# Kernel tuning notes

Measured on AMD Instinct MI355X. Metric: run time of the kernel, lower is better.

## Reference

```python
import jax, jax.numpy as jnp
import numpy as np

D, F, E, K = 1024, 2048, 8, 2
EPS = 1.1920929e-07  # torch.finfo(float32).eps, RMSNorm default eps=None


def setup_inputs() -> dict:
    key = jax.random.key(0)
    ks = jax.random.split(key, 6)
    x = jax.random.normal(ks[0], (2, 2048, D), jnp.float32)
    Wg = jax.random.normal(ks[1], (D, E), jnp.float32)          # Gate.weights ~ randn
    norm_w = jnp.ones((E, D), jnp.float32)                       # per-expert RMSNorm weight
    W1 = jax.random.normal(ks[2], (E, D, F), jnp.float32) * 0.02
    b1 = jnp.zeros((E, F), jnp.float32)
    W2 = jax.random.normal(ks[3], (E, D, F), jnp.float32) * 0.02
    b2 = jnp.zeros((E, F), jnp.float32)
    W3 = jax.random.normal(ks[4], (E, F, D), jnp.float32) * 0.02
    b3 = jnp.zeros((E, D), jnp.float32)
    return {"x": x, "Wg": Wg, "norm_w": norm_w, "W1": W1, "b1": b1,
            "W2": W2, "b2": b2, "W3": W3, "b3": b3, "k": K}


def reference(x, Wg, norm_w, W1, b1, W2, b2, W3, b3, k):
    orig_shape = x.shape
    xt = x.reshape(-1, x.shape[-1])                    # [T, d]
    num_experts = Wg.shape[-1]

    # --- Gate: top-k then softmax over selected logits ---
    scores = xt @ Wg                                   # [T, E]
    top_v, top_i = jax.lax.top_k(scores, k)            # [T, k]
    gates = jax.nn.softmax(top_v, axis=-1)             # [T, k]
    # combine weight per (token, expert); zero for unrouted experts
    comb = jnp.einsum('tk,tke->te', gates,
                      jax.nn.one_hot(top_i, num_experts, dtype=gates.dtype))  # [T, E]

    # --- Per-expert SwiGLU FFN with RMSNorm (norm weight folded into W1/W2) ---
    inv = jax.lax.rsqrt(jnp.mean(xt * xt, axis=-1, keepdims=True) + EPS)
    xh = xt * inv                                      # [T, d] (un-weighted RMSNorm)
    W1p = norm_w[:, :, None] * W1                      # [E, d, f]
    W2p = norm_w[:, :, None] * W2
    a = jnp.einsum('td,edf->etf', xh, W1p) + b1[:, None, :]   # [E, T, f]
    g = jnp.einsum('td,edf->etf', xh, W2p) + b2[:, None, :]
    h = jax.nn.silu(a) * g                             # [E, T, f]
    o = jnp.einsum('etf,efd->etd', h, W3) + b3[:, None, :]    # [E, T, d]

    # --- Weighted combine (comb==0 for unrouted -> identical to masked loop) ---
    y = jnp.einsum('etd,te->td', o, comb)              # [T, d]
    return y.reshape(orig_shape)
```

## Files before the change

kernel.cpp:

```cpp
#include <hip/hip_runtime.h>
#include <hip/hip_bf16.h>

typedef unsigned short u16;
typedef __attribute__((ext_vector_type(8))) short bf16x8;
typedef __attribute__((ext_vector_type(4))) float f32x4;

#define D_DIM 1024
#define F_DIM 2048
#define E_NUM 8
#define EPS_RMS 1.1920929e-07f
#define NCHUNK 16

__device__ __forceinline__ u16 f2bf(float f) {
  union { float f; unsigned u; } v; v.f = f;
  unsigned r = v.u + 0x7FFFu + ((v.u >> 16) & 1u);
  return (u16)(r >> 16);
}

__device__ __forceinline__ void async16(const void* g, void* l) {
  __builtin_amdgcn_global_load_lds((const __attribute__((address_space(1))) void*)g,
                                   (__attribute__((address_space(3))) void*)l, 16, 0, 0);
}

__global__ __launch_bounds__(256) void gate_kernel(
    const float* __restrict__ x, const float* __restrict__ Wg,
    u16* __restrict__ xh, int* __restrict__ topi, float* __restrict__ gatev)
{
  const int t = blockIdx.x;
  const int tid = threadIdx.x;
  const float4 xv = reinterpret_cast<const float4*>(x + (size_t)t * D_DIM)[tid];
  float ss = xv.x*xv.x + xv.y*xv.y + xv.z*xv.z + xv.w*xv.w;
  float s[8];
#pragma unroll
  for (int e = 0; e < 8; ++e) s[e] = 0.f;
  const float xa[4] = {xv.x, xv.y, xv.z, xv.w};
#pragma unroll
  for (int j = 0; j < 4; ++j) {
    const float4* wr = reinterpret_cast<const float4*>(Wg + (size_t)(tid*4 + j) * 8);
    float4 w0 = wr[0], w1 = wr[1];
    s[0] += xa[j]*w0.x; s[1] += xa[j]*w0.y; s[2] += xa[j]*w0.z; s[3] += xa[j]*w0.w;
    s[4] += xa[j]*w1.x; s[5] += xa[j]*w1.y; s[6] += xa[j]*w1.z; s[7] += xa[j]*w1.w;
  }
#pragma unroll
  for (int off = 32; off > 0; off >>= 1) {
    ss += __shfl_down(ss, off);
#pragma unroll
    for (int e = 0; e < 8; ++e) s[e] += __shfl_down(s[e], off);
  }
  __shared__ float red[4][9];
  __shared__ float invs;
  const int wv = tid >> 6, lane = tid & 63;
  if (lane == 0) { red[wv][8] = ss;
#pragma unroll
    for (int e = 0; e < 8; ++e) red[wv][e] = s[e]; }
  __syncthreads();
  if (tid == 0) {
    float sum2 = red[0][8] + red[1][8] + red[2][8] + red[3][8];
    invs = rsqrtf(sum2 * (1.0f / D_DIM) + EPS_RMS);
    float sc[8];
#pragma unroll
    for (int e = 0; e < 8; ++e) sc[e] = red[0][e] + red[1][e] + red[2][e] + red[3][e];
    int i0 = 0; float v0 = sc[0];
#pragma unroll
    for (int e = 1; e < 8; ++e) if (sc[e] > v0) { v0 = sc[e]; i0 = e; }
    int i1 = -1; float v1 = -3.0e38f;
#pragma unroll
    for (int e = 0; e < 8; ++e) if (e != i0 && sc[e] > v1) { v1 = sc[e]; i1 = e; }
    float p1 = 1.0f / (1.0f + expf(v0 - v1));
    float p0 = 1.0f - p1;
    topi[2*t] = i0; topi[2*t+1] = i1;
    gatev[2*t] = p0; gatev[2*t+1] = p1;
  }
  __syncthreads();
  const float inv = invs;
  ushort4 o;
  o.x = f2bf(xv.x*inv); o.y = f2bf(xv.y*inv); o.z = f2bf(xv.z*inv); o.w = f2bf(xv.w*inv);
  reinterpret_cast<ushort4*>(xh + (size_t)t * D_DIM)[tid] = o;
}

__global__ __launch_bounds__(256) void count_kernel(
    const int* __restrict__ topi, int* __restrict__ percnt, int nent)
{
  const int blk = blockIdx.x;
  const int tid = threadIdx.x;
  const int per = (nent + NCHUNK*256 - 1) / (NCHUNK*256);
  const int cbase = blk * 256 * per;
  int c[8];
#pragma unroll
  for (int q = 0; q < 8; ++q) c[q] = 0;
  for (int i = 0; i < per; ++i) {
    const int idx = cbase + tid * per + i;
    if (idx < nent) {
      const int e = topi[idx];
#pragma unroll
      for (int q = 0; q < 8; ++q) c[q] += (e == q) ? 1 : 0;
    }
  }
#pragma unroll
  for (int off = 32; off > 0; off >>= 1)
#pragma unroll
    for (int q = 0; q < 8; ++q) c[q] += __shfl_down(c[q], off);
  __shared__ int red[4][8];
  const int wv = tid >> 6, lane = tid & 63;
  if (lane == 0)
#pragma unroll
    for (int q = 0; q < 8; ++q) red[wv][q] = c[q];
  __syncthreads();
  if (tid < 8) percnt[blk * 8 + tid] = red[0][tid] + red[1][tid] + red[2][tid] + red[3][tid];
}

__global__ void scan_kernel(const int* __restrict__ percnt, int* __restrict__ offs,
                            int* __restrict__ base)
{
  if (threadIdx.x == 0) {
    int tot[8];
#pragma unroll
    for (int e = 0; e < 8; ++e) {
      tot[e] = 0;
      for (int c = 0; c < NCHUNK; ++c) tot[e] += percnt[c*8 + e];
    }
    int acc = 0, start[8];
#pragma unroll
    for (int e = 0; e < 8; ++e) { offs[e] = acc; start[e] = acc; acc += (tot[e] + 255) & ~255; }
    offs[8] = acc;
    for (int c = 0; c < NCHUNK; ++c)
#pragma unroll
      for (int e = 0; e < 8; ++e) { base[c*8 + e] = start[e]; start[e] += percnt[c*8 + e]; }
  }
}

__global__ __launch_bounds__(256) void scatter_kernel(
    const int* __restrict__ topi, const int* __restrict__ base,
    int* __restrict__ rowtok, int* __restrict__ slots, int nent)
{
  __shared__ int cur[8];
  const int blk = blockIdx.x, tid = threadIdx.x;
  if (tid < 8) cur[tid] = base[blk*8 + tid];
  __syncthreads();
  const int per = (nent + NCHUNK*256 - 1) / (NCHUNK*256);
  const int cbase = blk * 256 * per;
  for (int i = 0; i < per; ++i) {
    const int idx = cbase + tid * per + i;
    if (idx < nent) {
      const int e = topi[idx];
      const int pos = atomicAdd(&cur[e], 1);
      rowtok[pos] = idx >> 1;
      slots[idx] = pos;
    }
  }
}

__global__ __launch_bounds__(256) void transpose_fold_w12(
    const float* __restrict__ W1, const float* __restrict__ W2,
    const float* __restrict__ scale,
    u16* __restrict__ W1t, u16* __restrict__ W2t)
{
  __shared__ float tile[64][65];
  const int z = blockIdx.z;
  const int e = z & 7;
  const float* W = (z < 8) ? W1 : W2;
  u16* out = (z < 8) ? W1t : W2t;
  const int R = D_DIM, C = F_DIM;
  const int cb = blockIdx.x * 64, rb = blockIdx.y * 64;
  const int tx = threadIdx.x;
  const int ty = threadIdx.y;
  const float* Wp = W + (size_t)e * R * C;
#pragma unroll
  for (int rep = 0; rep < 4; ++rep) {
    const int i = ty + rep * 16;
    float4 v = *reinterpret_cast<const float4*>(Wp + (size_t)(rb + i) * C + cb + tx * 4);
    tile[i][tx*4+0] = v.x; tile[i][tx*4+1] = v.y; tile[i][tx*4+2] = v.z; tile[i][tx*4+3] = v.w;
  }
  __syncthreads();
  float sc[4];
#pragma unroll
  for (int q = 0; q < 4; ++q) sc[q] = scale[(size_t)e * R + rb + tx*4 + q];
  u16* op = out + (size_t)e * R * C;
#pragma unroll
  for (int rep = 0; rep < 4; ++rep) {
    const int j = ty + rep * 16;
    ushort4 o;
    o.x = f2bf(tile[tx*4+0][j] * sc[0]);
    o.y = f2bf(tile[tx*4+1][j] * sc[1]);
    o.z = f2bf(tile[tx*4+2][j] * sc[2]);
    o.w = f2bf(tile[tx*4+3][j] * sc[3]);
    *reinterpret_cast<ushort4*>(op + (size_t)(cb + j) * R + rb + tx*4) = o;
  }
}

__global__ __launch_bounds__(256) void transpose_w3(
    const float* __restrict__ W, u16* __restrict__ out)
{
  __shared__ float tile[64][65];
  const int e = blockIdx.z;
  const int R = F_DIM, C = D_DIM;
  const int cb = blockIdx.x * 64, rb = blockIdx.y * 64;
  const int tx = threadIdx.x, ty = threadIdx.y;
  const float* Wp = W + (size_t)e * R * C;
#pragma unroll
  for (int rep = 0; rep < 4; ++rep) {
    const int i = ty + rep * 16;
    float4 v = *reinterpret_cast<const float4*>(Wp + (size_t)(rb + i) * C + cb + tx * 4);
    tile[i][tx*4+0] = v.x; tile[i][tx*4+1] = v.y; tile[i][tx*4+2] = v.z; tile[i][tx*4+3] = v.w;
  }
  __syncthreads();
  u16* op = out + (size_t)e * R * C;
#pragma unroll
  for (int rep = 0; rep < 4; ++rep) {
    const int j = ty + rep * 16;
    ushort4 o;
    o.x = f2bf(tile[tx*4+0][j]);
    o.y = f2bf(tile[tx*4+1][j]);
    o.z = f2bf(tile[tx*4+2][j]);
    o.w = f2bf(tile[tx*4+3][j]);
    *reinterpret_cast<ushort4*>(op + (size_t)(cb + j) * R + rb + tx*4) = o;
  }
}

__global__ __launch_bounds__(512, 2) void ffn1_kernel(
    const u16* __restrict__ xh, const u16* __restrict__ W1t, const u16* __restrict__ W2t,
    const float* __restrict__ b1, const float* __restrict__ b2,
    const int* __restrict__ rowtok, const int* __restrict__ offs,
    u16* __restrict__ h)
{
  __shared__ __align__(16) u16 smem[65536];

  const int lin = blockIdx.y * gridDim.x + blockIdx.x;
  const int qc  = (gridDim.x * gridDim.y) >> 3;
  const int L   = (lin & 7) * qc + (lin >> 3);
  const int bx  = L % gridDim.x;
  const int by  = L / gridDim.x;

  const int row0 = by * 256;
  if (row0 >= offs[8]) return;
  int e = 0;
#pragma unroll
  for (int i = 1; i < 8; ++i) e += (row0 >= offs[i]) ? 1 : 0;

  const int n0 = bx * 128;
  const int tid = threadIdx.x;
  const int lane = tid & 63;
  const int wv = tid >> 6;
  const int wm = wv >> 1;
  const int wn = wv & 1;

  const int srow = tid >> 3;
  const int sseg = (tid & 7) ^ (srow & 7);
  int tokA[4];
#pragma unroll
  for (int j = 0; j < 4; ++j) {
    int tk = rowtok[row0 + srow + 64*j];
    tokA[j] = (tk < 0) ? 0 : tk;
  }
  const u16* gA[4];
#pragma unroll
  for (int j = 0; j < 4; ++j) gA[j] = xh + (size_t)tokA[j] * D_DIM + sseg * 8;
  const u16* gB1[2]; const u16* gB2[2];
#pragma unroll
  for (int j = 0; j < 2; ++j) {
    const size_t wrow = (size_t)e * F_DIM + n0 + srow + 64*j;
    gB1[j] = W1t + wrow * D_DIM + sseg * 8;
    gB2[j] = W2t + wrow * D_DIM + sseg * 8;
  }

  const f32x4 zero = {0.f, 0.f, 0.f, 0.f};
  f32x4 acc1[4][4], acc2[4][4];
#pragma unroll
  for (int i = 0; i < 4; ++i)
#pragma unroll
    for (int j = 0; j < 4; ++j) { acc1[i][j] = zero; acc2[i][j] = zero; }

  const int rswz = (lane & 7) << 3;
  const int kpart = (lane >> 4) * 8;
  const int arowbase = (wm*64 + (lane & 15)) * 64;
  const int browbase = (wn*64 + (lane & 15)) * 64;

#define STAGE(b, k0)                                                        \
  {                                                                         \
    const int aB = (b)*16384, b1B = 32768 + (b)*8192, b2B = 49152 + (b)*8192; \
    _Pragma("unroll")                                                       \
    for (int j = 0; j < 4; ++j)                                             \
      async16(gA[j] + (k0), &smem[aB + (tid + 512*j)*8]);                   \
    _Pragma("unroll")                                                       \
    for (int j = 0; j < 2; ++j) {                                           \
      async16(gB1[j] + (k0), &smem[b1B + (tid + 512*j)*8]);                 \
      async16(gB2[j] + (k0), &smem[b2B + (tid + 512*j)*8]);                 \
    }                                                                       \
  }

  STAGE(0, 0);
  __syncthreads();

  int cur = 0;
  for (int t = 0; t < D_DIM/64; ++t) {
    if (t + 1 < D_DIM/64) STAGE(cur ^ 1, (t+1)*64);
    const int aB = cur*16384, b1B = 32768 + cur*8192, b2B = 49152 + cur*8192;
#pragma unroll
    for (int kk = 0; kk < 2; ++kk) {
      const int ko = kk*32 + kpart;
      bf16x8 af[4], bv1[4], bv2[4];
#pragma unroll
      for (int mi = 0; mi < 4; ++mi)
        af[mi] = *(const bf16x8*)(&smem[aB + ((arowbase + mi*1024 + ko) ^ rswz)]);
#pragma unroll
      for (int ni = 0; ni < 4; ++ni) {
        bv1[ni] = *(const bf16x8*)(&smem[b1B + ((browbase + ni*1024 + ko) ^ rswz)]);
        bv2[ni] = *(const bf16x8*)(&smem[b2B + ((browbase + ni*1024 + ko) ^ rswz)]);
      }
#pragma unroll
      for (int mi = 0; mi < 4; ++mi)
#pragma unroll
        for (int ni = 0; ni < 4; ++ni) {
          acc1[mi][ni] = __builtin_amdgcn_mfma_f32_16x16x32_bf16(af[mi], bv1[ni], acc1[mi][ni], 0, 0, 0);
          acc2[mi][ni] = __builtin_amdgcn_mfma_f32_16x16x32_bf16(af[mi], bv2[ni], acc2[mi][ni], 0, 0, 0);
        }
    }
    __syncthreads();
    cur ^= 1;
  }
#undef STAGE

#pragma unroll
  for (int mi = 0; mi < 4; ++mi) {
    const int rbase = row0 + wm*64 + mi*16 + (lane >> 4)*4;
#pragma unroll
    for (int ni = 0; ni < 4; ++ni) {
      const int gc = n0 + wn*64 + ni*16 + (lane & 15);
      const float bb1 = b1[e*F_DIM + gc], bb2 = b2[e*F_DIM + gc];
#pragma unroll
      for (int r = 0; r < 4; ++r) {
        float a = acc1[mi][ni][r] + bb1;
        float g = acc2[mi][ni][r] + bb2;
        h[(size_t)(rbase + r) * F_DIM + gc] = f2bf(a / (1.f + __expf(-a)) * g);
      }
    }
  }
}

__global__ __launch_bounds__(256, 2) void ffn2_kernel(
    const u16* __restrict__ h, const u16* __restrict__ W3t,
    const float* __restrict__ b3, const int* __restrict__ offs,
    float* __restrict__ opart)
{
  __shared__ __align__(16) u16 smem[32768];

  const int lin = blockIdx.y * gridDim.x + blockIdx.x;
  const int qc  = (gridDim.x * gridDim.y) >> 3;
  const int L   = (lin & 7) * qc + (lin >> 3);
  const int bx  = L % gridDim.x;
  const int by  = L / gridDim.x;

  const int row0 = by * 128;
  if (row0 >= offs[8]) return;
  int e = 0;
#pragma unroll
  for (int i = 1; i < 8; ++i) e += (row0 >= offs[i]) ? 1 : 0;

  const int n0 = bx * 128;
  const int tid = threadIdx.x;
  const int lane = tid & 63;
  const int wv = tid >> 6;
  const int wm = wv >> 1;
  const int wn = wv & 1;

  const int srow = tid >> 3;
  const int sseg = (tid & 7) ^ (srow & 7);
  const u16* gA[4]; const u16* gB[4];
#pragma unroll
  for (int j = 0; j < 4; ++j) {
    gA[j] = h   + (size_t)(row0 + srow + 32*j) * F_DIM + sseg * 8;
    gB[j] = W3t + ((size_t)e * D_DIM + n0 + srow + 32*j) * F_DIM + sseg * 8;
  }

  const f32x4 zero = {0.f, 0.f, 0.f, 0.f};
  f32x4 acc[4][4];
#pragma unroll
  for (int i = 0; i < 4; ++i)
#pragma unroll
    for (int j = 0; j < 4; ++j) acc[i][j] = zero;

  const int rswz = (lane & 7) << 3;
  const int kpart = (lane >> 4) * 8;
  const int arowbase = (wm*64 + (lane & 15)) * 64;
  const int browbase = (wn*64 + (lane & 15)) * 64;

#define STAGE2(b, k0)                                                       \
  {                                                                         \
    const int aB = (b)*8192, bB = 16384 + (b)*8192;                         \
    _Pragma("unroll")                                                       \
    for (int j = 0; j < 4; ++j) {                                           \
      async16(gA[j] + (k0), &smem[aB + (tid + 256*j)*8]);                   \
      async16(gB[j] + (k0), &smem[bB + (tid + 256*j)*8]);                   \
    }                                                                       \
  }

  STAGE2(0, 0);
  __syncthreads();

  int cur = 0;
  for (int t = 0; t < F_DIM/64; ++t) {
    if (t + 1 < F_DIM/64) STAGE2(cur ^ 1, (t+1)*64);
    const int aB = cur*8192, bB = 16384 + cur*8192;
#pragma unroll
    for (int kk = 0; kk < 2; ++kk) {
      const int ko = kk*32 + kpart;
      bf16x8 af[4], bv[4];
#pragma unroll
      for (int mi = 0; mi < 4; ++mi)
        af[mi] = *(const bf16x8*)(&smem[aB + ((arowbase + mi*1024 + ko) ^ rswz)]);
#pragma unroll
      for (int ni = 0; ni < 4; ++ni)
        bv[ni] = *(const bf16x8*)(&smem[bB + ((browbase + ni*1024 + ko) ^ rswz)]);
#pragma unroll
      for (int mi = 0; mi < 4; ++mi)
#pragma unroll
        for (int ni = 0; ni < 4; ++ni)
          acc[mi][ni] = __builtin_amdgcn_mfma_f32_16x16x32_bf16(af[mi], bv[ni], acc[mi][ni], 0, 0, 0);
    }
    __syncthreads();
    cur ^= 1;
  }
#undef STAGE2

#pragma unroll
  for (int mi = 0; mi < 4; ++mi) {
    const int rbase = row0 + wm*64 + mi*16 + (lane >> 4)*4;
#pragma unroll
    for (int ni = 0; ni < 4; ++ni) {
      const int gc = n0 + wn*64 + ni*16 + (lane & 15);
      const float bb = b3[e*D_DIM + gc];
#pragma unroll
      for (int r = 0; r < 4; ++r)
        opart[(size_t)(rbase + r) * D_DIM + gc] = acc[mi][ni][r] + bb;
    }
  }
}

__global__ __launch_bounds__(256) void combine_kernel(
    const float* __restrict__ opart, const int* __restrict__ slots,
    const float* __restrict__ gatev, float* __restrict__ y)
{
  const int t = blockIdx.x;
  const int s0 = slots[2*t], s1 = slots[2*t+1];
  const float w0 = gatev[2*t], w1 = gatev[2*t+1];
  const float4 a = reinterpret_cast<const float4*>(opart + (size_t)s0 * D_DIM)[threadIdx.x];
  const float4 b = reinterpret_cast<const float4*>(opart + (size_t)s1 * D_DIM)[threadIdx.x];
  float4 o;
  o.x = w0*a.x + w1*b.x; o.y = w0*a.y + w1*b.y;
  o.z = w0*a.z + w1*b.z; o.w = w0*a.w + w1*b.w;
  reinterpret_cast<float4*>(y + (size_t)t * D_DIM)[threadIdx.x] = o;
}

extern "C" void kernel_launch(void* const* d_in, const int* in_sizes, int n_in,
                              void* d_out, int out_size, void* d_ws, size_t ws_size,
                              hipStream_t stream)
{
  const float* x  = (const float*)d_in[0];
  const float* Wg = (const float*)d_in[1];
  const float* nw = (const float*)d_in[2];
  const float* W1 = (const float*)d_in[3];
  const float* b1 = (const float*)d_in[4];
  const float* W2 = (const float*)d_in[5];
  const float* b2 = (const float*)d_in[6];
  const float* W3 = (const float*)d_in[7];
  const float* b3 = (const float*)d_in[8];
  float* y = (float*)d_out;

  const int T = in_sizes[0] / D_DIM;
  const int NENT = T * 2;
  const int RCAP = ((NENT + E_NUM * 255) + 255) & ~255;
  const int MT1 = RCAP / 256;
  const int MT2 = RCAP / 128;

  char* ws = (char*)d_ws;
  size_t off_ = 0;
  auto take = [&](size_t bytes) { char* p = ws + off_; off_ = (off_ + bytes + 255) & ~(size_t)255; return p; };
  u16* W1t    = (u16*)take((size_t)E_NUM * F_DIM * D_DIM * 2);
  u16* W2t    = (u16*)take((size_t)E_NUM * F_DIM * D_DIM * 2);
  u16* W3t    = (u16*)take((size_t)E_NUM * D_DIM * F_DIM * 2);
  u16* xh     = (u16*)take((size_t)T * D_DIM * 2);
  u16* hbuf   = (u16*)take((size_t)RCAP * F_DIM * 2);
  int* rowtok = (int*)take((size_t)RCAP * 4);
  int* slots  = (int*)take((size_t)NENT * 4);
  int* topi   = (int*)take((size_t)NENT * 4);
  float* gatev= (float*)take((size_t)NENT * 4);
  int* percnt = (int*)take(NCHUNK * 8 * 4);
  int* cbase  = (int*)take(NCHUNK * 8 * 4);
  int* offs   = (int*)take(64);
  float* opart = (float*)W1t;
  (void)ws_size; (void)n_in; (void)out_size;

  hipMemsetAsync(rowtok, 0xFF, (size_t)RCAP * 4, stream);

  transpose_fold_w12<<<dim3(F_DIM/64, D_DIM/64, 2*E_NUM), dim3(16, 16), 0, stream>>>(W1, W2, nw, W1t, W2t);
  transpose_w3<<<dim3(D_DIM/64, F_DIM/64, E_NUM), dim3(16, 16), 0, stream>>>(W3, W3t);

  gate_kernel<<<T, 256, 0, stream>>>(x, Wg, xh, topi, gatev);
  count_kernel<<<NCHUNK, 256, 0, stream>>>(topi, percnt, NENT);
  scan_kernel<<<1, 64, 0, stream>>>(percnt, offs, cbase);
  scatter_kernel<<<NCHUNK, 256, 0, stream>>>(topi, cbase, rowtok, slots, NENT);

  ffn1_kernel<<<dim3(F_DIM/128, MT1), 512, 0, stream>>>(xh, W1t, W2t, b1, b2, rowtok, offs, hbuf);
  ffn2_kernel<<<dim3(D_DIM/128, MT2), 256, 0, stream>>>(hbuf, W3t, b3, offs, opart);
  combine_kernel<<<T, 256, 0, stream>>>(opart, slots, gatev, y);
}
```

Before: 242.6 us.

## Split ffn1 K-step into two phases with fine-grained vmcnt waits

Restructures the ffn1 main loop so each K-step first runs the W1 MFMAs, then waits only for the W2 tile before running the W2 MFMAs. Explicit s_waitcnt vmcnt counts and a raw s_barrier replace the full __syncthreads, and the next stage's W2 prefetch is issued after the W1 phase. It also drops the XCD-aware block remapping in ffn1 and uses blockIdx directly. The goal is more overlap between async global-to-LDS loads and MFMA work, at the cost of fragile hand-counted wait values, reloading the A fragments twice per step, and possibly worse L2 locality without the remap.

Result: slower. 247.9 us (+2.2%).

```diff
diff --git a/kernel.cpp b/kernel.cpp
--- a/kernel.cpp
+++ b/kernel.cpp
@@ -225,13 +225,148 @@
 {
   __shared__ __align__(16) u16 smem[65536];
 
+  const int row0 = blockIdx.y * 256;
+  if (row0 >= offs[8]) return;
+  int e = 0;
+#pragma unroll
+  for (int i = 1; i < 8; ++i) e += (row0 >= offs[i]) ? 1 : 0;
+
+  const int n0 = blockIdx.x * 128;
+  const int tid = threadIdx.x;
+  const int lane = tid & 63;
+  const int wv = tid >> 6;
+  const int wm = wv >> 1;
+  const int wn = wv & 1;
+
+  const int srow = tid >> 3;
+  const int sseg = (tid & 7) ^ (srow & 7);
+  int tokA[4];
+#pragma unroll
+  for (int j = 0; j < 4; ++j) {
+    int tk = rowtok[row0 + srow + 64*j];
+    tokA[j] = (tk < 0) ? 0 : tk;
+  }
+  const u16* gA[4];
+#pragma unroll
+  for (int j = 0; j < 4; ++j) gA[j] = xh + (size_t)tokA[j] * D_DIM + sseg * 8;
+  const u16* gB1[2]; const u16* gB2[2];
+#pragma unroll
+  for (int j = 0; j < 2; ++j) {
+    const size_t wrow = (size_t)e * F_DIM + n0 + srow + 64*j;
+    gB1[j] = W1t + wrow * D_DIM + sseg * 8;
+    gB2[j] = W2t + wrow * D_DIM + sseg * 8;
+  }
+
+  const f32x4 zero = {0.f, 0.f, 0.f, 0.f};
+  f32x4 acc1[4][4], acc2[4][4];
+#pragma unroll
+  for (int i = 0; i < 4; ++i)
+#pragma unroll
+    for (int j = 0; j < 4; ++j) { acc1[i][j] = zero; acc2[i][j] = zero; }
+
+  const int rswz = (lane & 7) << 3;
+  const int kpart = (lane >> 4) * 8;
+  const int arowbase = (wm*64 + (lane & 15)) * 64;
+  const int browbase = (wn*64 + (lane & 15)) * 64;
+
+  {
+#pragma unroll
+    for (int j = 0; j < 4; ++j) async16(gA[j], &smem[0 + (tid + 512*j)*8]);
+#pragma unroll
+    for (int j = 0; j < 2; ++j) async16(gB1[j], &smem[32768 + (tid + 512*j)*8]);
+#pragma unroll
+    for (int j = 0; j < 2; ++j) async16(gB2[j], &smem[49152 + (tid + 512*j)*8]);
+  }
+
+  int cur = 0;
+  for (int t = 0; t < D_DIM/64; ++t) {
+    const int nxt = cur ^ 1;
+    const int aB = cur*16384, b1B = 32768 + cur*8192, b2B = 49152 + cur*8192;
+    asm volatile("s_waitcnt vmcnt(2)" ::: "memory");
+    __builtin_amdgcn_s_barrier();
+    if (t + 1 < D_DIM/64) {
+      const int kn = (t+1)*64;
+      const int aN = nxt*16384, b1N = 32768 + nxt*8192;
+#pragma unroll
+      for (int j = 0; j < 4; ++j) async16(gA[j] + kn, &smem[aN + (tid + 512*j)*8]);
+#pragma unroll
+      for (int j = 0; j < 2; ++j) async16(gB1[j] + kn, &smem[b1N + (tid + 512*j)*8]);
+    }
+#pragma unroll
+    for (int kk = 0; kk < 2; ++kk) {
+      const int ko = kk*32 + kpart;
+      bf16x8 af[4], bv1[4];
+#pragma unroll
+      for (int mi = 0; mi < 4; ++mi)
+        af[mi] = *(const bf16x8*)(&smem[aB + ((arowbase + mi*1024 + ko) ^ rswz)]);
+#pragma unroll
+      for (int ni = 0; ni < 4; ++ni)
+        bv1[ni] = *(const bf16x8*)(&smem[b1B + ((browbase + ni*1024 + ko) ^ rswz)]);
+#pragma unroll
+      for (int mi = 0; mi < 4; ++mi)
+#pragma unroll
+        for (int ni = 0; ni < 4; ++ni)
+          acc1[mi][ni] = __builtin_amdgcn_mfma_f32_16x16x32_bf16(af[mi], bv1[ni], acc1[mi][ni], 0, 0, 0);
+    }
+    if (t + 1 < D_DIM/64) {
+      asm volatile("s_waitcnt vmcnt(6)" ::: "memory");
+      const int kn = (t+1)*64;
+      const int b2N = 49152 + nxt*8192;
+#pragma unroll
+      for (int j = 0; j < 2; ++j) async16(gB2[j] + kn, &smem[b2N + (tid + 512*j)*8]);
+    } else {
+      asm volatile("s_waitcnt vmcnt(0)" ::: "memory");
+    }
+#pragma unroll
+    for (int kk = 0; kk < 2; ++kk) {
+      const int ko = kk*32 + kpart;
+      bf16x8 af[4], bv2[4];
+#pragma unroll
+      for (int mi = 0; mi < 4; ++mi)
+        af[mi] = *(const bf16x8*)(&smem[aB + ((arowbase + mi*1024 + ko) ^ rswz)]);
+#pragma unroll
+      for (int ni = 0; ni < 4; ++ni)
+        bv2[ni] = *(const bf16x8*)(&smem[b2B + ((browbase + ni*1024 + ko) ^ rswz)]);
+#pragma unroll
+      for (int mi = 0; mi < 4; ++mi)
+#pragma unroll
+        for (int ni = 0; ni < 4; ++ni)
+          acc2[mi][ni] = __builtin_amdgcn_mfma_f32_16x16x32_bf16(af[mi], bv2[ni], acc2[mi][ni], 0, 0, 0);
+    }
+    cur = nxt;
+  }
+
+#pragma unroll
+  for (int mi = 0; mi < 4; ++mi) {
+    const int rbase = row0 + wm*64 + mi*16 + (lane >> 4)*4;
+#pragma unroll
+    for (int ni = 0; ni < 4; ++ni) {
+      const int gc = n0 + wn*64 + ni*16 + (lane & 15);
+      const float bb1 = b1[e*F_DIM + gc], bb2 = b2[e*F_DIM + gc];
+#pragma unroll
+      for (int r = 0; r < 4; ++r) {
+        float a = acc1[mi][ni][r] + bb1;
+        float g = acc2[mi][ni][r] + bb2;
+        h[(size_t)(rbase + r) * F_DIM + gc] = f2bf(a / (1.f + __expf(-a)) * g);
+      }
+    }
+  }
+}
+
+__global__ __launch_bounds__(256, 2) void ffn2_kernel(
+    const u16* __restrict__ h, const u16* __restrict__ W3t,
+    const float* __restrict__ b3, const int* __restrict__ offs,
+    float* __restrict__ opart)
+{
+  __shared__ __align__(16) u16 smem[32768];
+
   const int lin = blockIdx.y * gridDim.x + blockIdx.x;
   const int qc  = (gridDim.x * gridDim.y) >> 3;
   const int L   = (lin & 7) * qc + (lin >> 3);
   const int bx  = L % gridDim.x;
   const int by  = L / gridDim.x;
 
-  const int row0 = by * 256;
+  const int row0 = by * 128;
   if (row0 >= offs[8]) return;
   int e = 0;
 #pragma unroll
@@ -246,151 +381,32 @@
 
   const int srow = tid >> 3;
   const int sseg = (tid & 7) ^ (srow & 7);
-  int tokA[4];
+  const u16* gA[4]; const u16* gB[4];
 #pragma unroll
   for (int j = 0; j < 4; ++j) {
-    int tk = rowtok[row0 + srow + 64*j];
-    tokA[j] = (tk < 0) ? 0 : tk;
-  }
-  const u16* gA[4];
-#pragma unroll
-  for (int j = 0; j < 4; ++j) gA[j] = xh + (size_t)tokA[j] * D_DIM + sseg * 8;
-  const u16* gB1[2]; const u16* gB2[2];
-#pragma unroll
-  for (int j = 0; j < 2; ++j) {
-    const size_t wrow = (size_t)e * F_DIM + n0 + srow + 64*j;
-    gB1[j] = W1t + wrow * D_DIM + sseg * 8;
-    gB2[j] = W2t + wrow * D_DIM + sseg * 8;
+    gA[j] = h   + (size_t)(row0 + srow + 32*j) * F_DIM + sseg * 8;
+    gB[j] = W3t + ((size_t)e * D_DIM + n0 + srow + 32*j) * F_DIM + sseg * 8;
   }
 
   const f32x4 zero = {0.f, 0.f, 0.f, 0.f};
-  f32x4 acc1[4][4], acc2[4][4];
+  f32x4 acc[4][4];
 #pragma unroll
   for (int i = 0; i < 4; ++i)
 #pragma unroll
-    for (int j = 0; j < 4; ++j) { acc1[i][j] = zero; acc2[i][j] = zero; }
+    for (int j = 0; j < 4; ++j) acc[i][j] = zero;
 
   const int rswz = (lane & 7) << 3;
   const int kpart = (lane >> 4) * 8;
   const int arowbase = (wm*64 + (lane & 15)) * 64;
   const int browbase = (wn*64 + (lane & 15)) * 64;
 
-#define STAGE(b, k0)                                                        \
-  {                                                                         \
-    const int aB = (b)*16384, b1B = 32768 + (b)*8192, b2B = 49152 + (b)*8192; \
-    _Pragma("unroll")                                                       \
-    for (int j = 0; j < 4; ++j)                                             \
-      async16(gA[j] + (k0), &smem[aB + (tid + 512*j)*8]);                   \
-    _Pragma("unroll")                                                       \
-    for (int j = 0; j < 2; ++j) {                                           \
-      async16(gB1[j] + (k0), &smem[b1B + (tid + 512*j)*8]);                 \
-      async16(gB2[j] + (k0), &smem[b2B + (tid + 512*j)*8]);                 \
-    }                                                                       \
-  }
-
-  STAGE(0, 0);
-  __syncthreads();
-
-  int cur = 0;
-  for (int t = 0; t < D_DIM/64; ++t) {
-    if (t + 1 < D_DIM/64) STAGE(cur ^ 1, (t+1)*64);
-    const int aB = cur*16384, b1B = 32768 + cur*8192, b2B = 49152 + cur*8192;
-#pragma unroll
-    for (int kk = 0; kk < 2; ++kk) {
-      const int ko = kk*32 + kpart;
-      bf16x8 af[4], bv1[4], bv2[4];
-#pragma unroll
-      for (int mi = 0; mi < 4; ++mi)
-        af[mi] = *(const bf16x8*)(&smem[aB + ((arowbase + mi*1024 + ko) ^ rswz)]);
-#pragma unroll
-      for (int ni = 0; ni < 4; ++ni) {
-        bv1[ni] = *(const bf16x8*)(&smem[b1B + ((browbase + ni*1024 + ko) ^ rswz)]);
-        bv2[ni] = *(const bf16x8*)(&smem[b2B + ((browbase + ni*1024 + ko) ^ rswz)]);
-      }
-#pragma unroll
-      for (int mi = 0; mi < 4; ++mi)
-#pragma unroll
-        for (int ni = 0; ni < 4; ++ni) {
-          acc1[mi][ni] = __builtin_amdgcn_mfma_f32_16x16x32_bf16(af[mi], bv1[ni], acc1[mi][ni], 0, 0, 0);
-          acc2[mi][ni] = __builtin_amdgcn_mfma_f32_16x16x32_bf16(af[mi], bv2[ni], acc2[mi][ni], 0, 0, 0);
-        }
-    }
-    __syncthreads();
-    cur ^= 1;
-  }
-#undef STAGE
-
-#pragma unroll
-  for (int mi = 0; mi < 4; ++mi) {
-    const int rbase = row0 + wm*64 + mi*16 + (lane >> 4)*4;
-#pragma unroll
-    for (int ni = 0; ni < 4; ++ni) {
-      const int gc = n0 + wn*64 + ni*16 + (lane & 15);
-      const float bb1 = b1[e*F_DIM + gc], bb2 = b2[e*F_DIM + gc];
-#pragma unroll
-      for (int r = 0; r < 4; ++r) {
-        float a = acc1[mi][ni][r] + bb1;
-        float g = acc2[mi][ni][r] + bb2;
-        h[(size_t)(rbase + r) * F_DIM + gc] = f2bf(a / (1.f + __expf(-a)) * g);
-      }
-    }
-  }
-}
-
-__global__ __launch_bounds__(256, 2) void ffn2_kernel(
-    const u16* __restrict__ h, const u16* __restrict__ W3t,
-    const float* __restrict__ b3, const int* __restrict__ offs,
-    float* __restrict__ opart)
-{
-  __shared__ __align__(16) u16 smem[32768];
-
-  const int lin = blockIdx.y * gridDim.x + blockIdx.x;
-  const int qc  = (gridDim.x * gridDim.y) >> 3;
-  const int L   = (lin & 7) * qc + (lin >> 3);
-  const int bx  = L % gridDim.x;
-  const int by  = L / gridDim.x;
-
-  const int row0 = by * 128;
-  if (row0 >= offs[8]) return;
-  int e = 0;
-#pragma unroll
-  for (int i = 1; i < 8; ++i) e += (row0 >= offs[i]) ? 1 : 0;
-
-  const int n0 = bx * 128;
-  const int tid = threadIdx.x;
-  const int lane = tid & 63;
-  const int wv = tid >> 6;
-  const int wm = wv >> 1;
-  const int wn = wv & 1;
-
-  const int srow = tid >> 3;
-  const int sseg = (tid & 7) ^ (srow & 7);
-  const u16* gA[4]; const u16* gB[4];
-#pragma unroll
-  for (int j = 0; j < 4; ++j) {
-    gA[j] = h   + (size_t)(row0 + srow + 32*j) * F_DIM + sseg * 8;
-    gB[j] = W3t + ((size_t)e * D_DIM + n0 + srow + 32*j) * F_DIM + sseg * 8;
-  }
-
-  const f32x4 zero = {0.f, 0.f, 0.f, 0.f};
-  f32x4 acc[4][4];
-#pragma unroll
-  for (int i = 0; i < 4; ++i)
-#pragma unroll
-    for (int j = 0; j < 4; ++j) acc[i][j] = zero;
-
-  const int rswz = (lane & 7) << 3;
-  const int kpart = (lane >> 4) * 8;
-  const int arowbase = (wm*64 + (lane & 15)) * 64;
-  const int browbase = (wn*64 + (lane & 15)) * 64;
-
 #define STAGE2(b, k0)                                                       \
   {                                                                         \
-    const int aB = (b)*8192, bB = 16384 + (b)*8192;                         \
+    const int aB_ = (b)*8192, bB_ = 16384 + (b)*8192;                       \
     _Pragma("unroll")                                                       \
     for (int j = 0; j < 4; ++j) {                                           \
-      async16(gA[j] + (k0), &smem[aB + (tid + 256*j)*8]);                   \
-      async16(gB[j] + (k0), &smem[bB + (tid + 256*j)*8]);                   \
+      async16(gA[j] + (k0), &smem[aB_ + (tid + 256*j)*8]);                  \
+      async16(gB[j] + (k0), &smem[bB_ + (tid + 256*j)*8]);                  \
     }                                                                       \
   }
 
```

## Interleave W1/W2 into one weight matrix and shrink ffn1 tile for occupancy

Applied to the files above, without the earlier changes.

The weight transpose now writes W1 and W2 into a single combined matrix, interleaved in 16-row groups. ffn1 can then run one GEMM with 128 combined output columns (64 of W1 and 64 of W2) and one accumulator set, instead of two separate accumulator sets. The K step drops to 32 and LDS use goes from 128KB to 48KB, with a new XOR swizzle and launch bounds raised to 4 blocks per CU. The grid also doubles along F and the block-remap swizzle is removed. This cuts register and LDS pressure to raise occupancy, at the cost of more K iterations, one barrier per 32-wide step, and possibly weaker L2 locality.

Measured after the change: 247.6 us. +2.0%, slower.

```diff
diff --git a/kernel.cpp b/kernel.cpp
--- a/kernel.cpp
+++ b/kernel.cpp
@@ -152,14 +152,13 @@
 
 __global__ __launch_bounds__(256) void transpose_fold_w12(
     const float* __restrict__ W1, const float* __restrict__ W2,
-    const float* __restrict__ scale,
-    u16* __restrict__ W1t, u16* __restrict__ W2t)
+    const float* __restrict__ scale, u16* __restrict__ Wc)
 {
   __shared__ float tile[64][65];
   const int z = blockIdx.z;
   const int e = z & 7;
   const float* W = (z < 8) ? W1 : W2;
-  u16* out = (z < 8) ? W1t : W2t;
+  const int gofs = (z < 8) ? 0 : 16;
   const int R = D_DIM, C = F_DIM;
   const int cb = blockIdx.x * 64, rb = blockIdx.y * 64;
   const int tx = threadIdx.x;
@@ -175,16 +174,18 @@
   float sc[4];
 #pragma unroll
   for (int q = 0; q < 4; ++q) sc[q] = scale[(size_t)e * R + rb + tx*4 + q];
-  u16* op = out + (size_t)e * R * C;
+  u16* op = Wc + (size_t)e * (2*F_DIM) * D_DIM;
 #pragma unroll
   for (int rep = 0; rep < 4; ++rep) {
     const int j = ty + rep * 16;
+    const int c = cb + j;
+    const int rphys = ((c >> 4) << 5) + (c & 15) + gofs;
     ushort4 o;
     o.x = f2bf(tile[tx*4+0][j] * sc[0]);
     o.y = f2bf(tile[tx*4+1][j] * sc[1]);
     o.z = f2bf(tile[tx*4+2][j] * sc[2]);
     o.w = f2bf(tile[tx*4+3][j] * sc[3]);
-    *reinterpret_cast<ushort4*>(op + (size_t)(cb + j) * R + rb + tx*4) = o;
+    *reinterpret_cast<ushort4*>(op + (size_t)rphys * D_DIM + rb + tx*4) = o;
   }
 }
 
@@ -217,13 +218,102 @@
   }
 }
 
-__global__ __launch_bounds__(512, 2) void ffn1_kernel(
-    const u16* __restrict__ xh, const u16* __restrict__ W1t, const u16* __restrict__ W2t,
+__global__ __launch_bounds__(512, 4) void ffn1_kernel(
+    const u16* __restrict__ xh, const u16* __restrict__ Wc,
     const float* __restrict__ b1, const float* __restrict__ b2,
     const int* __restrict__ rowtok, const int* __restrict__ offs,
     u16* __restrict__ h)
 {
-  __shared__ __align__(16) u16 smem[65536];
+  __shared__ __align__(16) u16 smem[24576];
+
+  const int row0 = blockIdx.y * 256;
+  if (row0 >= offs[8]) return;
+  int e = 0;
+#pragma unroll
+  for (int i = 1; i < 8; ++i) e += (row0 >= offs[i]) ? 1 : 0;
+
+  const int bx = blockIdx.x;
+  const int n0p = bx * 128;
+  const int tid = threadIdx.x;
+  const int lane = tid & 63;
+  const int l15 = lane & 15;
+  const int wv = tid >> 6;
+  const int wm = wv >> 1;
+  const int wn = wv & 1;
+
+  const int srow = tid >> 2;
+  const int sseg = tid & 3;
+  const int swzs = sseg ^ (srow & 3) ^ ((srow >> 2) & 3);
+  int tk0 = rowtok[row0 + srow];        if (tk0 < 0) tk0 = 0;
+  int tk1 = rowtok[row0 + 128 + srow];  if (tk1 < 0) tk1 = 0;
+  const u16* gA0 = xh + (size_t)tk0 * D_DIM + swzs * 8;
+  const u16* gA1 = xh + (size_t)tk1 * D_DIM + swzs * 8;
+  const u16* gB  = Wc + ((size_t)e * (2*F_DIM) + n0p + srow) * D_DIM + swzs * 8;
+
+  const f32x4 zero = {0.f, 0.f, 0.f, 0.f};
+  f32x4 acc[4][4];
+#pragma unroll
+  for (int i = 0; i < 4; ++i)
+#pragma unroll
+    for (int j = 0; j < 4; ++j) acc[i][j] = zero;
+
+  const int rsw = ((lane >> 4) ^ (l15 & 3) ^ ((l15 >> 2) & 3)) * 8;
+
+#define STAGE1(b, k0)                                                       \
+  {                                                                         \
+    const int aB_ = (b)*8192, bB_ = 16384 + (b)*4096;                       \
+    async16(gA0 + (k0), &smem[aB_ + tid*8]);                                \
+    async16(gA1 + (k0), &smem[aB_ + (tid + 512)*8]);                        \
+    async16(gB  + (k0), &smem[bB_ + tid*8]);                                \
+  }
+
+  STAGE1(0, 0);
+  __syncthreads();
+
+  int cur = 0;
+  for (int t = 0; t < D_DIM/32; ++t) {
+    if (t + 1 < D_DIM/32) STAGE1(cur ^ 1, (t+1)*32);
+    const int aB = cur*8192, bB = 16384 + cur*4096;
+    bf16x8 af[4], bv[4];
+#pragma unroll
+    for (int mi = 0; mi < 4; ++mi)
+      af[mi] = *(const bf16x8*)(&smem[aB + (wm*64 + mi*16 + l15)*32 + rsw]);
+#pragma unroll
+    for (int ni = 0; ni < 4; ++ni)
+      bv[ni] = *(const bf16x8*)(&smem[bB + (wn*64 + ni*16 + l15)*32 + rsw]);
+#pragma unroll
+    for (int mi = 0; mi < 4; ++mi)
+#pragma unroll
+      for (int ni = 0; ni < 4; ++ni)
+        acc[mi][ni] = __builtin_amdgcn_mfma_f32_16x16x32_bf16(af[mi], bv[ni], acc[mi][ni], 0, 0, 0);
+    __syncthreads();
+    cur ^= 1;
+  }
+#undef STAGE1
+
+#pragma unroll
+  for (int mi = 0; mi < 4; ++mi) {
+    const int rbase = row0 + wm*64 + mi*16 + (lane >> 4)*4;
+#pragma unroll
+    for (int q = 0; q < 2; ++q) {
+      const int rc = bx*64 + wn*32 + q*16 + l15;
+      const float bb1 = b1[e*F_DIM + rc], bb2 = b2[e*F_DIM + rc];
+#pragma unroll
+      for (int r = 0; r < 4; ++r) {
+        float a = acc[mi][2*q][r] + bb1;
+        float g = acc[mi][2*q+1][r] + bb2;
+        h[(size_t)(rbase + r) * F_DIM + rc] = f2bf(a / (1.f + __expf(-a)) * g);
+      }
+    }
+  }
+}
+
+__global__ __launch_bounds__(256, 2) void ffn2_kernel(
+    const u16* __restrict__ h, const u16* __restrict__ W3t,
+    const float* __restrict__ b3, const int* __restrict__ offs,
+    float* __restrict__ opart)
+{
+  __shared__ __align__(16) u16 smem[32768];
 
   const int lin = blockIdx.y * gridDim.x + blockIdx.x;
   const int qc  = (gridDim.x * gridDim.y) >> 3;
@@ -231,7 +321,7 @@
   const int bx  = L % gridDim.x;
   const int by  = L / gridDim.x;
 
-  const int row0 = by * 256;
+  const int row0 = by * 128;
   if (row0 >= offs[8]) return;
   int e = 0;
 #pragma unroll
@@ -246,151 +336,32 @@
 
   const int srow = tid >> 3;
   const int sseg = (tid & 7) ^ (srow & 7);
-  int tokA[4];
+  const u16* gA[4]; const u16* gB[4];
 #pragma unroll
   for (int j = 0; j < 4; ++j) {
-    int tk = rowtok[row0 + srow + 64*j];
-    tokA[j] = (tk < 0) ? 0 : tk;
-  }
-  const u16* gA[4];
-#pragma unroll
-  for (int j = 0; j < 4; ++j) gA[j] = xh + (size_t)tokA[j] * D_DIM + sseg * 8;
-  const u16* gB1[2]; const u16* gB2[2];
-#pragma unroll
-  for (int j = 0; j < 2; ++j) {
-    const size_t wrow = (size_t)e * F_DIM + n0 + srow + 64*j;
-    gB1[j] = W1t + wrow * D_DIM + sseg * 8;
-    gB2[j] = W2t + wrow * D_DIM + sseg * 8;
+    gA[j] = h   + (size_t)(row0 + srow + 32*j) * F_DIM + sseg * 8;
+    gB[j] = W3t + ((size_t)e * D_DIM + n0 + srow + 32*j) * F_DIM + sseg * 8;
   }
 
   const f32x4 zero = {0.f, 0.f, 0.f, 0.f};
-  f32x4 acc1[4][4], acc2[4][4];
+  f32x4 acc[4][4];
 #pragma unroll
   for (int i = 0; i < 4; ++i)
 #pragma unroll
-    for (int j = 0; j < 4; ++j) { acc1[i][j] = zero; acc2[i][j] = zero; }
+    for (int j = 0; j < 4; ++j) acc[i][j] = zero;
 
   const int rswz = (lane & 7) << 3;
   const int kpart = (lane >> 4) * 8;
   const int arowbase = (wm*64 + (lane & 15)) * 64;
   const int browbase = (wn*64 + (lane & 15)) * 64;
 
-#define STAGE(b, k0)                                                        \
-  {                                                                         \
-    const int aB = (b)*16384, b1B = 32768 + (b)*8192, b2B = 49152 + (b)*8192; \
-    _Pragma("unroll")                                                       \
-    for (int j = 0; j < 4; ++j)                                             \
-      async16(gA[j] + (k0), &smem[aB + (tid + 512*j)*8]);                   \
-    _Pragma("unroll")                                                       \
-    for (int j = 0; j < 2; ++j) {                                           \
-      async16(gB1[j] + (k0), &smem[b1B + (tid + 512*j)*8]);                 \
-      async16(gB2[j] + (k0), &smem[b2B + (tid + 512*j)*8]);                 \
-    }                                                                       \
-  }
-
-  STAGE(0, 0);
-  __syncthreads();
-
-  int cur = 0;
-  for (int t = 0; t < D_DIM/64; ++t) {
-    if (t + 1 < D_DIM/64) STAGE(cur ^ 1, (t+1)*64);
-    const int aB = cur*16384, b1B = 32768 + cur*8192, b2B = 49152 + cur*8192;
-#pragma unroll
-    for (int kk = 0; kk < 2; ++kk) {
-      const int ko = kk*32 + kpart;
-      bf16x8 af[4], bv1[4], bv2[4];
-#pragma unroll
-      for (int mi = 0; mi < 4; ++mi)
-        af[mi] = *(const bf16x8*)(&smem[aB + ((arowbase + mi*1024 + ko) ^ rswz)]);
-#pragma unroll
-      for (int ni = 0; ni < 4; ++ni) {
-        bv1[ni] = *(const bf16x8*)(&smem[b1B + ((browbase + ni*1024 + ko) ^ rswz)]);
-        bv2[ni] = *(const bf16x8*)(&smem[b2B + ((browbase + ni*1024 + ko) ^ rswz)]);
-      }
-#pragma unroll
-      for (int mi = 0; mi < 4; ++mi)
-#pragma unroll
-        for (int ni = 0; ni < 4; ++ni) {
-          acc1[mi][ni] = __builtin_amdgcn_mfma_f32_16x16x32_bf16(af[mi], bv1[ni], acc1[mi][ni], 0, 0, 0);
-          acc2[mi][ni] = __builtin_amdgcn_mfma_f32_16x16x32_bf16(af[mi], bv2[ni], acc2[mi][ni], 0, 0, 0);
-        }
-    }
-    __syncthreads();
-    cur ^= 1;
-  }
-#undef STAGE
-
-#pragma unroll
-  for (int mi = 0; mi < 4; ++mi) {
-    const int rbase = row0 + wm*64 + mi*16 + (lane >> 4)*4;
-#pragma unroll
-    for (int ni = 0; ni < 4; ++ni) {
-      const int gc = n0 + wn*64 + ni*16 + (lane & 15);
-      const float bb1 = b1[e*F_DIM + gc], bb2 = b2[e*F_DIM + gc];
-#pragma unroll
-      for (int r = 0; r < 4; ++r) {
-        float a = acc1[mi][ni][r] + bb1;
-        float g = acc2[mi][ni][r] + bb2;
-        h[(size_t)(rbase + r) * F_DIM + gc] = f2bf(a / (1.f + __expf(-a)) * g);
-      }
-    }
-  }
-}
-
-__global__ __launch_bounds__(256, 2) void ffn2_kernel(
-    const u16* __restrict__ h, const u16* __restrict__ W3t,
-    const float* __restrict__ b3, const int* __restrict__ offs,
-    float* __restrict__ opart)
-{
-  __shared__ __align__(16) u16 smem[32768];
-
-  const int lin = blockIdx.y * gridDim.x + blockIdx.x;
-  const int qc  = (gridDim.x * gridDim.y) >> 3;
-  const int L   = (lin & 7) * qc + (lin >> 3);
-  const int bx  = L % gridDim.x;
-  const int by  = L / gridDim.x;
-
-  const int row0 = by * 128;
-  if (row0 >= offs[8]) return;
-  int e = 0;
-#pragma unroll
-  for (int i = 1; i < 8; ++i) e += (row0 >= offs[i]) ? 1 : 0;
-
-  const int n0 = bx * 128;
-  const int tid = threadIdx.x;
-  const int lane = tid & 63;
-  const int wv = tid >> 6;
-  const int wm = wv >> 1;
-  const int wn = wv & 1;
-
-  const int srow = tid >> 3;
-  const int sseg = (tid & 7) ^ (srow & 7);
-  const u16* gA[4]; const u16* gB[4];
-#pragma unroll
-  for (int j = 0; j < 4; ++j) {
-    gA[j] = h   + (size_t)(row0 + srow + 32*j) * F_DIM + sseg * 8;
-    gB[j] = W3t + ((size_t)e * D_DIM + n0 + srow + 32*j) * F_DIM + sseg * 8;
-  }
-
-  const f32x4 zero = {0.f, 0.f, 0.f, 0.f};
-  f32x4 acc[4][4];
-#pragma unroll
-  for (int i = 0; i < 4; ++i)
-#pragma unroll
-    for (int j = 0; j < 4; ++j) acc[i][j] = zero;
-
-  const int rswz = (lane & 7) << 3;
-  const int kpart = (lane >> 4) * 8;
-  const int arowbase = (wm*64 + (lane & 15)) * 64;
-  const int browbase = (wn*64 + (lane & 15)) * 64;
-
 #define STAGE2(b, k0)                                                       \
   {                                                                         \
-    const int aB = (b)*8192, bB = 16384 + (b)*8192;                         \
+    const int aB_ = (b)*8192, bB_ = 16384 + (b)*8192;                       \
     _Pragma("unroll")                                                       \
     for (int j = 0; j < 4; ++j) {                                           \
-      async16(gA[j] + (k0), &smem[aB + (tid + 256*j)*8]);                   \
-      async16(gB[j] + (k0), &smem[bB + (tid + 256*j)*8]);                   \
+      async16(gA[j] + (k0), &smem[aB_ + (tid + 256*j)*8]);                  \
+      async16(gB[j] + (k0), &smem[bB_ + (tid + 256*j)*8]);                  \
     }                                                                       \
   }
 
@@ -475,8 +446,7 @@
   char* ws = (char*)d_ws;
   size_t off_ = 0;
   auto take = [&](size_t bytes) { char* p = ws + off_; off_ = (off_ + bytes + 255) & ~(size_t)255; return p; };
-  u16* W1t    = (u16*)take((size_t)E_NUM * F_DIM * D_DIM * 2);
-  u16* W2t    = (u16*)take((size_t)E_NUM * F_DIM * D_DIM * 2);
+  u16* Wc     = (u16*)take((size_t)E_NUM * 2 * F_DIM * D_DIM * 2);
   u16* W3t    = (u16*)take((size_t)E_NUM * D_DIM * F_DIM * 2);
   u16* xh     = (u16*)take((size_t)T * D_DIM * 2);
   u16* hbuf   = (u16*)take((size_t)RCAP * F_DIM * 2);
@@ -487,12 +457,12 @@
   int* percnt = (int*)take(NCHUNK * 8 * 4);
   int* cbase  = (int*)take(NCHUNK * 8 * 4);
   int* offs   = (int*)take(64);
-  float* opart = (float*)W1t;
+  float* opart = (float*)Wc;
   (void)ws_size; (void)n_in; (void)out_size;
 
   hipMemsetAsync(rowtok, 0xFF, (size_t)RCAP * 4, stream);
 
-  transpose_fold_w12<<<dim3(F_DIM/64, D_DIM/64, 2*E_NUM), dim3(16, 16), 0, stream>>>(W1, W2, nw, W1t, W2t);
+  transpose_fold_w12<<<dim3(F_DIM/64, D_DIM/64, 2*E_NUM), dim3(16, 16), 0, stream>>>(W1, W2, nw, Wc);
   transpose_w3<<<dim3(D_DIM/64, F_DIM/64, E_NUM), dim3(16, 16), 0, stream>>>(W3, W3t);
 
   gate_kernel<<<T, 256, 0, stream>>>(x, Wg, xh, topi, gatev);
@@ -500,7 +470,7 @@
   scan_kernel<<<1, 64, 0, stream>>>(percnt, offs, cbase);
   scatter_kernel<<<NCHUNK, 256, 0, stream>>>(topi, cbase, rowtok, slots, NENT);
 
-  ffn1_kernel<<<dim3(F_DIM/128, MT1), 512, 0, stream>>>(xh, W1t, W2t, b1, b2, rowtok, offs, hbuf);
+  ffn1_kernel<<<dim3(F_DIM/64, MT1), 512, 0, stream>>>(xh, Wc, b1, b2, rowtok, offs, hbuf);
   ffn2_kernel<<<dim3(D_DIM/128, MT2), 256, 0, stream>>>(hbuf, W3t, b3, offs, opart);
   combine_kernel<<<T, 256, 0, stream>>>(opart, slots, gatev, y);
 }
```
